# Kernel tuning notes

Hardware: AMD Instinct MI355X
Metric: run time of the kernel (lower is better)

## Reference

```python
import jax, jax.numpy as jnp
import numpy as np

B, G, K, H, NC = 128, 12000, 512, 64, 100
FP = 2048
ALPHA = 0.1
STEPS = 10

def setup_inputs() -> dict:
    key = jax.random.key(0)
    ks = jax.random.split(key, 10)
    ctl = jax.random.normal(ks[0], (B, G), jnp.float32)
    # drug targets: sparse binary indicator per gene
    drug_targets = (jax.random.uniform(ks[1], (B, G)) < 0.01).astype(jnp.float32)
    cell_idx = jax.random.randint(ks[2], (B,), 0, NC, dtype=jnp.int32)
    drug_fp = jax.random.normal(ks[3], (B, FP), jnp.float32)  # unused in forward
    # gene->module membership (sparse-ish binary), ensure each module non-empty via deg clamp in model
    M = (jax.random.uniform(ks[4], (G, K)) < 0.02).astype(jnp.float32)
    # row-stochastic module adjacency for stable diffusion
    Araw = jax.random.uniform(ks[5], (K, K), jnp.float32)
    A = Araw / jnp.sum(Araw, axis=1, keepdims=True)
    W_in = jax.random.normal(ks[6], (2, H), jnp.float32) * 0.5
    b_in = jnp.zeros((H,), jnp.float32)
    cell_emb = jax.random.normal(ks[7], (NC, H), jnp.float32) * 0.02
    W_out = jax.random.normal(ks[8], (H, 1), jnp.float32) * 0.1
    b_out = jnp.zeros((1,), jnp.float32)
    return {"ctl": ctl, "drug_targets": drug_targets, "cell_idx": cell_idx,
            "drug_fp": drug_fp, "M": M, "A": A, "W_in": W_in, "b_in": b_in,
            "cell_emb": cell_emb, "W_out": W_out, "b_out": b_out}

def reference(ctl, drug_targets, cell_idx, drug_fp, M, A, W_in, b_in, cell_emb, W_out, b_out):
    # module degree (clamped) as in __init__
    mod_deg = jnp.maximum(jnp.sum(M, axis=0), 1.0)            # [K]
    x_gene = jnp.stack([ctl, drug_targets], axis=-1)          # [B,G,2]
    x_mod = jnp.einsum('gk,bgh->bkh', M, x_gene) / mod_deg[None, :, None]  # [B,K,2]
    S = jax.nn.relu(x_mod @ W_in + b_in)                      # [B,K,H]
    # 10-step personalized-PageRank-style diffusion over modules
    def step(Z, _):
        Z = (1.0 - ALPHA) * jnp.einsum('bkh,kl->blh', Z, A) + ALPHA * S
        return Z, None
    Z, _ = jax.lax.scan(step, S, None, length=STEPS)          # [B,K,H]
    h_gene = jnp.einsum('gk,bkh->bgh', M, Z)                  # [B,G,H]
    h_gene = h_gene + cell_emb[cell_idx][:, None, :]          # add cell embedding
    y = (h_gene @ W_out + b_out)[..., 0]                      # [B,G]
    return y
```

## Files before the change

kernel.cpp:

```cpp
#include <hip/hip_runtime.h>

#define B_    128
#define G_    12000
#define GP    12288
#define K_    512
#define H_    64
#define NSEG  24
#define SEGG  512
#define BKT   64

typedef __attribute__((ext_vector_type(8))) short bf16x8;
typedef __attribute__((ext_vector_type(4))) float f32x4;

__device__ __forceinline__ unsigned short f2bf(float x) {
    union { float f; unsigned u; } v; v.f = x;
    unsigned r = (v.u + 0x7FFFu + ((v.u >> 16) & 1u)) >> 16;
    return (unsigned short)r;
}
__device__ __forceinline__ float bf2f(unsigned short b) {
    union { float f; unsigned u; } v; v.u = ((unsigned)b) << 16;
    return v.f;
}

__device__ __forceinline__ void mm_body(int k0, int l0, float* __restrict__ sm,
        const float* __restrict__ Aop, const float* __restrict__ Bop,
        const float* __restrict__ Cop, const float* __restrict__ Dop,
        float alpha, float beta, float* __restrict__ O, float* __restrict__ O2) {
    float (*Xa)[68] = (float(*)[68])sm;
    float (*Xb)[36] = (float(*)[36])(sm + 2176);
    int tid = threadIdx.x;
    int kg = tid & 15, lg = tid >> 4;
    float acc[2][2] = {};
    for (int jj = 0; jj < K_; jj += 64) {
#pragma unroll
        for (int i = 0; i < 2; ++i) {
            int lin = tid + i * 256;
            int r = lin >> 4, c4 = lin & 15;
            *(float4*)&Xa[r][c4 * 4] =
                *(const float4*)&Aop[(size_t)(l0 + r) * K_ + jj + c4 * 4];
        }
#pragma unroll
        for (int i = 0; i < 2; ++i) {
            int lin = tid + i * 256;
            int r = lin >> 3, c4 = lin & 7;
            *(float4*)&Xb[r][c4 * 4] =
                *(const float4*)&Bop[(size_t)(jj + r) * K_ + k0 + c4 * 4];
        }
        __syncthreads();
#pragma unroll 8
        for (int j = 0; j < 64; ++j) {
            float xa0 = Xa[lg * 2][j], xa1 = Xa[lg * 2 + 1][j];
            float xb0 = Xb[j][kg * 2], xb1 = Xb[j][kg * 2 + 1];
            acc[0][0] = fmaf(xa0, xb0, acc[0][0]);
            acc[0][1] = fmaf(xa0, xb1, acc[0][1]);
            acc[1][0] = fmaf(xa1, xb0, acc[1][0]);
            acc[1][1] = fmaf(xa1, xb1, acc[1][1]);
        }
        __syncthreads();
    }
#pragma unroll
    for (int i = 0; i < 2; ++i) {
        size_t idx = (size_t)(l0 + lg * 2 + i) * K_ + k0 + kg * 2;
        float2 v;
        v.x = alpha * acc[i][0];
        v.y = alpha * acc[i][1];
        if (beta != 0.0f) {
            float2 cc = *(const float2*)&Cop[idx];
            v.x = fmaf(beta, cc.x, v.x);
            v.y = fmaf(beta, cc.y, v.y);
        }
        *(float2*)&O[idx] = v;
        if (O2) {
            float2 dd = *(const float2*)&Dop[idx];
            float2 w2; w2.x = v.x + dd.x; w2.y = v.y + dd.y;
            *(float2*)&O2[idx] = w2;
        }
    }
}

__global__ __launch_bounds__(256) void k_pre(
        const float* __restrict__ ctl, const float* __restrict__ dt,
        const float* __restrict__ M, const float* __restrict__ A,
        const int* __restrict__ cidx, const float* __restrict__ cemb,
        const float* __restrict__ W_out, const float* __restrict__ b_out,
        unsigned short* __restrict__ XpT, unsigned short* __restrict__ MTb,
        unsigned short* __restrict__ Mb, int* __restrict__ deg,
        float* __restrict__ AT, float* __restrict__ U2,
        float* __restrict__ cvec) {
    int bid = blockIdx.x, tid = threadIdx.x;
    if (bid < 3072) {
        int p = bid / 12, chunk = bid % 12;
        int ch = p >> 7, b = p & 127;
        const float* src = (ch ? dt : ctl) + (size_t)b * G_;
        int g = chunk * 1024 + tid * 4;
        float x0 = 0.f, x1 = 0.f, x2 = 0.f, x3 = 0.f;
        if (g + 3 < G_) {
            float4 v = *(const float4*)&src[g];
            x0 = v.x; x1 = v.y; x2 = v.z; x3 = v.w;
        } else {
            if (g + 0 < G_) x0 = src[g + 0];
            if (g + 1 < G_) x1 = src[g + 1];
            if (g + 2 < G_) x2 = src[g + 2];
            if (g + 3 < G_) x3 = src[g + 3];
        }
        ushort4 hv;
        hv.x = f2bf(x0); hv.y = f2bf(x1); hv.z = f2bf(x2); hv.w = f2bf(x3);
        *(ushort4*)&XpT[(size_t)p * GP + g] = hv;
    } else if (bid < 4608) {
        __shared__ float t[64][65];
        __shared__ int csum[4][64];
        int id = bid - 3072;
        int gt = id % 192, kt = id / 192;
        int g0 = gt * 64, k0 = kt * 64;
        int tx = tid & 63, ty = tid >> 6;
        int cnt = 0;
#pragma unroll
        for (int j = 0; j < 16; ++j) {
            int g = g0 + ty + 4 * j;
            float v = (g < G_) ? M[(size_t)g * K_ + k0 + tx] : 0.0f;
            t[ty + 4 * j][tx] = v;
            Mb[(size_t)g * K_ + k0 + tx] = f2bf(v);
            cnt += (v != 0.0f);
        }
        csum[ty][tx] = cnt;
        __syncthreads();
        if (ty == 0)
            atomicAdd(&deg[k0 + tx],
                      csum[0][tx] + csum[1][tx] + csum[2][tx] + csum[3][tx]);
#pragma unroll
        for (int j = 0; j < 16; ++j)
            MTb[(size_t)(k0 + ty + 4 * j) * GP + g0 + tx] =
                f2bf(t[tx][ty + 4 * j]);
    } else if (bid < 4864) {
        __shared__ float t[32][33];
        int id = bid - 4608;
        int x0 = (id & 15) * 32, y0 = (id >> 4) * 32;
        int tx = tid & 31, ty = tid >> 5;
#pragma unroll
        for (int j = 0; j < 4; ++j)
            t[ty + 8 * j][tx] = A[(size_t)(y0 + ty + 8 * j) * K_ + x0 + tx];
        __syncthreads();
#pragma unroll
        for (int j = 0; j < 4; ++j) {
            int row = x0 + ty + 8 * j, col = y0 + tx;
            float v = t[tx][ty + 8 * j];
            AT[(size_t)row * K_ + col] = v;
            U2[(size_t)row * K_ + col] = 0.09f * v + (row == col ? 0.1f : 0.0f);
        }
    } else {
        if (tid < B_) {
            int ci = cidx[tid];
            float acc = b_out[0];
#pragma unroll 8
            for (int h = 0; h < H_; ++h)
                acc = fmaf(cemb[ci * H_ + h], W_out[h], acc);
            cvec[tid] = acc;
        }
    }
}

__global__ __launch_bounds__(256) void k_gemm(
        const unsigned short* __restrict__ MTb, const unsigned short* __restrict__ XpT,
        float* __restrict__ Cp,
        const float* __restrict__ AT, const float* __restrict__ U2,
        float* __restrict__ M2, float* __restrict__ Yop) {
    __shared__ __align__(16) char smraw[36864];
    int bid = blockIdx.x, tid = threadIdx.x;
    if (bid < 192) {
        unsigned short (*Al)[72] = (unsigned short(*)[72])smraw;
        unsigned short (*Bl)[72] = (unsigned short(*)[72])(smraw + 18432);
        int tile = bid & 7, seg = bid >> 3;
        int m0 = (tile & 3) * 128, n0 = (tile >> 2) * 128;
        size_t gbase = (size_t)seg * SEGG;
        int wid = tid >> 6, lane = tid & 63;
        int wm = (wid >> 1) * 64, wn = (wid & 1) * 64;
        int r16 = lane & 15, kg8 = (lane >> 4) * 8;
        int ld_row = tid >> 3, ld_c8 = (tid & 7) * 8;
        f32x4 acc[4][4] = {};
        for (int kk = 0; kk < SEGG; kk += BKT) {
#pragma unroll
            for (int i = 0; i < 4; ++i) {
                int r = ld_row + 32 * i;
                *(uint4*)&Al[r][ld_c8] =
                    *(const uint4*)&MTb[(size_t)(m0 + r) * GP + gbase + kk + ld_c8];
                *(uint4*)&Bl[r][ld_c8] =
                    *(const uint4*)&XpT[(size_t)(n0 + r) * GP + gbase + kk + ld_c8];
            }
            __syncthreads();
#pragma unroll
            for (int ks = 0; ks < 2; ++ks) {
                bf16x8 af[4], bf[4];
#pragma unroll
                for (int mi = 0; mi < 4; ++mi)
                    af[mi] = *(const bf16x8*)&Al[wm + mi * 16 + r16][ks * 32 + kg8];
#pragma unroll
                for (int ni = 0; ni < 4; ++ni)
                    bf[ni] = *(const bf16x8*)&Bl[wn + ni * 16 + r16][ks * 32 + kg8];
#pragma unroll
                for (int mi = 0; mi < 4; ++mi)
#pragma unroll
                    for (int ni = 0; ni < 4; ++ni)
                        acc[mi][ni] = __builtin_amdgcn_mfma_f32_16x16x32_bf16(
                            af[mi], bf[ni], acc[mi][ni], 0, 0, 0);
            }
            __syncthreads();
        }
        float* C = Cp + (size_t)seg * (K_ * 256);
        int cr = (lane >> 4) * 4, cc = lane & 15;
#pragma unroll
        for (int mi = 0; mi < 4; ++mi)
#pragma unroll
            for (int ni = 0; ni < 4; ++ni) {
                size_t rb = (size_t)(m0 + wm + mi * 16 + cr) * 256
                          + (n0 + wn + ni * 16 + cc);
#pragma unroll
                for (int r = 0; r < 4; ++r)
                    C[rb + (size_t)r * 256] = acc[mi][ni][r];
            }
    } else {
        int id = bid - 192;
        mm_body((id & 15) * 32, (id >> 4) * 32, (float*)smraw,
                AT, AT, nullptr, U2, 0.81f, 0.0f, M2, Yop);
    }
}

__global__ __launch_bounds__(256) void k_red(
        const float* __restrict__ Cp, const int* __restrict__ deg,
        const float* __restrict__ W_in, const float* __restrict__ b_in,
        const float* __restrict__ W_out, float* __restrict__ sout,
        const float* __restrict__ M2, const float* __restrict__ U2,
        float* __restrict__ M4, float* __restrict__ U4) {
    __shared__ __align__(16) float sm[4480];
    int bid = blockIdx.x, tid = threadIdx.x;
    if (bid < 256) {
        int kloc = tid >> 7, b = tid & 127;
        int k = bid * 2 + kloc;
        float x0 = 0.f, x1 = 0.f;
#pragma unroll 4
        for (int s = 0; s < NSEG; ++s) {
            const float* Cb = Cp + (size_t)s * (K_ * 256) + (size_t)k * 256;
            x0 += Cb[b];
            x1 += Cb[128 + b];
        }
        float inv = 1.0f / fmaxf((float)deg[k], 1.0f);
        x0 *= inv; x1 *= inv;
        float s = 0.f;
#pragma unroll 8
        for (int h = 0; h < H_; ++h) {
            float v = fmaf(x0, W_in[h], fmaf(x1, W_in[H_ + h], b_in[h]));
            v = fmaxf(v, 0.f);
            s = fmaf(v, W_out[h], s);
        }
        sout[k * B_ + b] = s;
    } else {
        int id = bid - 256;
        int t = id & 255;
        if (id < 256)
            mm_body((t & 15) * 32, (t >> 4) * 32, sm, M2, M2, nullptr, nullptr,
                    1.0f, 0.0f, M4, nullptr);
        else
            mm_body((t & 15) * 32, (t >> 4) * 32, sm, M2, U2, U2, nullptr,
                    1.0f, 1.0f, U4, nullptr);
    }
}

__global__ __launch_bounds__(256) void k_p3(
        const float* __restrict__ M4, const float* __restrict__ U4,
        float* __restrict__ M8, float* __restrict__ U8,
        const float* __restrict__ Yop, const float* __restrict__ sout,
        float* __restrict__ q) {
    __shared__ __align__(16) float sm[4480];
    int bid = blockIdx.x, tid = threadIdx.x;
    if (bid < 512) {
        int t = bid & 255;
        if (bid < 256)
            mm_body((t & 15) * 32, (t >> 4) * 32, sm, M4, M4, nullptr, nullptr,
                    1.0f, 0.0f, M8, nullptr);
        else
            mm_body((t & 15) * 32, (t >> 4) * 32, sm, M4, U4, U4, nullptr,
                    1.0f, 1.0f, U8, nullptr);
    } else {
        int l = bid - 512;
        float* Wr  = sm;
        float* red = sm + 512;
        if (tid < 128)
            ((float4*)Wr)[tid] = ((const float4*)&Yop[(size_t)l * K_])[tid];
        __syncthreads();
        int b = tid & 127, seg = tid >> 7;
        int kb = seg * 256;
        float a0 = 0.f, a1 = 0.f, a2 = 0.f, a3 = 0.f;
#pragma unroll 4
        for (int kk = 0; kk < 256; kk += 4) {
            int k = kb + kk;
            a0 = fmaf(Wr[k + 0], sout[(k + 0) * B_ + b], a0);
            a1 = fmaf(Wr[k + 1], sout[(k + 1) * B_ + b], a1);
            a2 = fmaf(Wr[k + 2], sout[(k + 2) * B_ + b], a2);
            a3 = fmaf(Wr[k + 3], sout[(k + 3) * B_ + b], a3);
        }
        red[seg * 128 + b] = (a0 + a1) + (a2 + a3);
        __syncthreads();
        if (tid < 128)
            q[l * B_ + b] = red[b] + red[128 + b];
    }
}

__global__ __launch_bounds__(1024) void k_zfin(
        const float* __restrict__ M8, const float* __restrict__ U8,
        const float* __restrict__ q, const float* __restrict__ sout,
        unsigned short* __restrict__ zbT) {
    __shared__ __align__(16) float Wr[4 * K_];
    __shared__ float red[8][2][128];
    int tid = threadIdx.x;
    int l0 = blockIdx.x * 2;
    if (tid < 256)
        ((float4*)Wr)[tid] = ((const float4*)&M8[(size_t)l0 * K_])[tid];
    else if (tid < 512)
        ((float4*)&Wr[2 * K_])[tid - 256] =
            ((const float4*)&U8[(size_t)l0 * K_])[tid - 256];
    __syncthreads();
    int b = tid & 127, seg = tid >> 7;
    int kb = seg * 64;
    float a0m = 0.f, a0u = 0.f, a1m = 0.f, a1u = 0.f;
#pragma unroll 8
    for (int kk = 0; kk < 64; ++kk) {
        int k = kb + kk;
        float qv = q[k * B_ + b];
        float sv = sout[k * B_ + b];
        a0m = fmaf(Wr[k], qv, a0m);
        a0u = fmaf(Wr[2 * K_ + k], sv, a0u);
        a1m = fmaf(Wr[K_ + k], qv, a1m);
        a1u = fmaf(Wr[3 * K_ + k], sv, a1u);
    }
    red[seg][0][b] = a0m + a0u;
    red[seg][1][b] = a1m + a1u;
    __syncthreads();
    if (tid < 256) {
        int row = tid >> 7, bb = tid & 127;
        float t = 0.f;
#pragma unroll
        for (int u = 0; u < 8; ++u) t += red[u][row][bb];
        unsigned short hi = f2bf(t);
        unsigned short lo = f2bf(t - bf2f(hi));
        zbT[(size_t)bb * (2 * K_) + (l0 + row)]      = hi;
        zbT[(size_t)bb * (2 * K_) + K_ + (l0 + row)] = lo;
    }
}

__global__ __launch_bounds__(256) void k_yg(
        const unsigned short* __restrict__ Mb, const unsigned short* __restrict__ zbT,
        const float* __restrict__ cvec, float* __restrict__ y) {
    __shared__ __align__(16) unsigned short Al[128][72];
    __shared__ __align__(16) unsigned short Bh[128][72];
    __shared__ __align__(16) unsigned short Bl2[128][72];
    int tid = threadIdx.x;
    int g0 = blockIdx.x * 128;
    int wid = tid >> 6, lane = tid & 63;
    int wm = (wid >> 1) * 64, wn = (wid & 1) * 64;
    int r16 = lane & 15, kg8 = (lane >> 4) * 8;
    int ld_row = tid >> 3, ld_c8 = (tid & 7) * 8;
    f32x4 acc[4][4] = {};
    for (int kk = 0; kk < K_; kk += BKT) {
#pragma unroll
        for (int i = 0; i < 4; ++i) {
            int r = ld_row + 32 * i;
            *(uint4*)&Al[r][ld_c8] =
                *(const uint4*)&Mb[(size_t)(g0 + r) * K_ + kk + ld_c8];
            *(uint4*)&Bh[r][ld_c8] =
                *(const uint4*)&zbT[(size_t)r * (2 * K_) + kk + ld_c8];
            *(uint4*)&Bl2[r][ld_c8] =
                *(const uint4*)&zbT[(size_t)r * (2 * K_) + K_ + kk + ld_c8];
        }
        __syncthreads();
#pragma unroll
        for (int ks = 0; ks < 2; ++ks) {
            bf16x8 af[4], bh[4], bl[4];
#pragma unroll
            for (int mi = 0; mi < 4; ++mi)
                af[mi] = *(const bf16x8*)&Al[wm + mi * 16 + r16][ks * 32 + kg8];
#pragma unroll
            for (int ni = 0; ni < 4; ++ni) {
                bh[ni] = *(const bf16x8*)&Bh[wn + ni * 16 + r16][ks * 32 + kg8];
                bl[ni] = *(const bf16x8*)&Bl2[wn + ni * 16 + r16][ks * 32 + kg8];
            }
#pragma unroll
            for (int mi = 0; mi < 4; ++mi)
#pragma unroll
                for (int ni = 0; ni < 4; ++ni) {
                    acc[mi][ni] = __builtin_amdgcn_mfma_f32_16x16x32_bf16(
                        af[mi], bh[ni], acc[mi][ni], 0, 0, 0);
                    acc[mi][ni] = __builtin_amdgcn_mfma_f32_16x16x32_bf16(
                        af[mi], bl[ni], acc[mi][ni], 0, 0, 0);
                }
        }
        __syncthreads();
    }
    int cr = (lane >> 4) * 4, cc = lane & 15;
#pragma unroll
    for (int ni = 0; ni < 4; ++ni) {
        int b = wn + ni * 16 + cc;
        float cv = cvec[b];
#pragma unroll
        for (int mi = 0; mi < 4; ++mi) {
            int g = g0 + wm + mi * 16 + cr;
            if (g < G_) {
                float4 o;
                o.x = acc[mi][ni][0] + cv;
                o.y = acc[mi][ni][1] + cv;
                o.z = acc[mi][ni][2] + cv;
                o.w = acc[mi][ni][3] + cv;
                *(float4*)&y[(size_t)b * G_ + g] = o;
            }
        }
    }
}

extern "C" void kernel_launch(void* const* d_in, const int* in_sizes, int n_in,
                              void* d_out, int out_size, void* d_ws, size_t ws_size,
                              hipStream_t stream) {
    const float* ctl   = (const float*)d_in[0];
    const float* dt    = (const float*)d_in[1];
    const int*   cidx  = (const int*)d_in[2];
    const float* M     = (const float*)d_in[4];
    const float* A     = (const float*)d_in[5];
    const float* W_in  = (const float*)d_in[6];
    const float* b_in  = (const float*)d_in[7];
    const float* cemb  = (const float*)d_in[8];
    const float* W_out = (const float*)d_in[9];
    const float* b_out = (const float*)d_in[10];
    float* y = (float*)d_out;

    char* ws = (char*)d_ws;
    size_t o = 0;
    auto take = [&](size_t bytes) { char* p = ws + o; o = (o + bytes + 255) & ~(size_t)255; return p; };
    unsigned short* XpT = (unsigned short*)take((size_t)256 * GP * 2);
    unsigned short* MTb = (unsigned short*)take((size_t)K_ * GP * 2);
    unsigned short* Mb  = (unsigned short*)take((size_t)GP * K_ * 2);
    unsigned short* zbT = (unsigned short*)take((size_t)B_ * 2 * K_ * 2);
    float* Cp   = (float*)take((size_t)NSEG * K_ * 256 * 4);
    int*   deg  = (int*)  take(K_ * 4);
    float* cvec = (float*)take(B_ * 4);
    float* AT   = (float*)take((size_t)K_ * K_ * 4);
    float* U2   = (float*)take((size_t)K_ * K_ * 4);
    float* M2   = (float*)take((size_t)K_ * K_ * 4);
    float* Yop  = (float*)take((size_t)K_ * K_ * 4);
    float* M4   = (float*)take((size_t)K_ * K_ * 4);
    float* U4   = (float*)take((size_t)K_ * K_ * 4);
    float* M8   = (float*)take((size_t)K_ * K_ * 4);
    float* U8   = (float*)take((size_t)K_ * K_ * 4);
    float* sout = (float*)take((size_t)K_ * B_ * 4);
    float* q    = (float*)take((size_t)K_ * B_ * 4);
    (void)ws_size; (void)in_sizes; (void)n_in; (void)out_size;

    hipMemsetAsync(deg, 0, K_ * 4, stream);
    k_pre<<<4865, 256, 0, stream>>>(ctl, dt, M, A, cidx, cemb, W_out, b_out,
                                    XpT, MTb, Mb, deg, AT, U2, cvec);
    k_gemm<<<448, 256, 0, stream>>>(MTb, XpT, Cp, AT, U2, M2, Yop);
    k_red<<<768, 256, 0, stream>>>(Cp, deg, W_in, b_in, W_out, sout,
                                   M2, U2, M4, U4);
    k_p3<<<1024, 256, 0, stream>>>(M4, U4, M8, U8, Yop, sout, q);
    k_zfin<<<K_ / 2, 1024, 0, stream>>>(M8, U8, q, sout, zbT);
    k_yg<<<(G_ + 127) / 128, 256, 0, stream>>>(Mb, zbT, cvec, y);
}
```

Measured before the change: 112.9 us.

## Replace U8 matmul with panel matvec, drop degree atomics, shrink final GEMM tile

The U8 = M4·U4 + U4 matrix-matrix product is replaced by a matrix-vector product (U4 applied to sout), and its result is folded into the final reduction in k_zfin together with M4. The module-degree atomics and the memset are replaced by per-tile partial counts written to a buffer and reduced inside k_red. The output GEMM tile is halved to 64 rows, doubling the number of blocks to improve occupancy across CUs. This trades one 512³ GEMM for cheaper matvecs, at the cost of more partial-degree traffic and a reassociated floating-point sum.

```diff
diff --git a/kernel.cpp b/kernel.cpp
--- a/kernel.cpp
+++ b/kernel.cpp
@@ -8,6 +8,7 @@
 #define NSEG  24
 #define SEGG  512
 #define BKT   64
+#define NGT   192
 
 typedef __attribute__((ext_vector_type(8))) short bf16x8;
 typedef __attribute__((ext_vector_type(4))) float f32x4;
@@ -78,13 +79,39 @@
     }
 }
 
+__device__ __forceinline__ void panel_body(int l, float* __restrict__ sm,
+        const float* __restrict__ W, const float* __restrict__ src,
+        float* __restrict__ out) {
+    float* Wr  = sm;
+    float* red = sm + 512;
+    int tid = threadIdx.x;
+    if (tid < 128)
+        ((float4*)Wr)[tid] = ((const float4*)&W[(size_t)l * K_])[tid];
+    __syncthreads();
+    int b = tid & 127, seg = tid >> 7;
+    int kb = seg * 256;
+    float a0 = 0.f, a1 = 0.f, a2 = 0.f, a3 = 0.f;
+#pragma unroll 4
+    for (int kk = 0; kk < 256; kk += 4) {
+        int k = kb + kk;
+        a0 = fmaf(Wr[k + 0], src[(k + 0) * B_ + b], a0);
+        a1 = fmaf(Wr[k + 1], src[(k + 1) * B_ + b], a1);
+        a2 = fmaf(Wr[k + 2], src[(k + 2) * B_ + b], a2);
+        a3 = fmaf(Wr[k + 3], src[(k + 3) * B_ + b], a3);
+    }
+    red[seg * 128 + b] = (a0 + a1) + (a2 + a3);
+    __syncthreads();
+    if (tid < 128)
+        out[l * B_ + b] = red[b] + red[128 + b];
+}
+
 __global__ __launch_bounds__(256) void k_pre(
         const float* __restrict__ ctl, const float* __restrict__ dt,
         const float* __restrict__ M, const float* __restrict__ A,
         const int* __restrict__ cidx, const float* __restrict__ cemb,
         const float* __restrict__ W_out, const float* __restrict__ b_out,
         unsigned short* __restrict__ XpT, unsigned short* __restrict__ MTb,
-        unsigned short* __restrict__ Mb, int* __restrict__ deg,
+        unsigned short* __restrict__ Mb, int* __restrict__ pdeg,
         float* __restrict__ AT, float* __restrict__ U2,
         float* __restrict__ cvec) {
     int bid = blockIdx.x, tid = threadIdx.x;
@@ -110,7 +137,7 @@
         __shared__ float t[64][65];
         __shared__ int csum[4][64];
         int id = bid - 3072;
-        int gt = id % 192, kt = id / 192;
+        int gt = id % NGT, kt = id / NGT;
         int g0 = gt * 64, k0 = kt * 64;
         int tx = tid & 63, ty = tid >> 6;
         int cnt = 0;
@@ -125,8 +152,8 @@
         csum[ty][tx] = cnt;
         __syncthreads();
         if (ty == 0)
-            atomicAdd(&deg[k0 + tx],
-                      csum[0][tx] + csum[1][tx] + csum[2][tx] + csum[3][tx]);
+            pdeg[(size_t)(k0 + tx) * NGT + gt] =
+                csum[0][tx] + csum[1][tx] + csum[2][tx] + csum[3][tx];
 #pragma unroll
         for (int j = 0; j < 16; ++j)
             MTb[(size_t)(k0 + ty + 4 * j) * GP + g0 + tx] =
@@ -225,7 +252,7 @@
 }
 
 __global__ __launch_bounds__(256) void k_red(
-        const float* __restrict__ Cp, const int* __restrict__ deg,
+        const float* __restrict__ Cp, const int* __restrict__ pdeg,
         const float* __restrict__ W_in, const float* __restrict__ b_in,
         const float* __restrict__ W_out, float* __restrict__ sout,
         const float* __restrict__ M2, const float* __restrict__ U2,
@@ -235,6 +262,17 @@
     if (bid < 256) {
         int kloc = tid >> 7, b = tid & 127;
         int k = bid * 2 + kloc;
+        int v = 0;
+        if (b < 96)
+            v = pdeg[(size_t)k * NGT + b] + pdeg[(size_t)k * NGT + 96 + b];
+#pragma unroll
+        for (int off = 32; off; off >>= 1) v += __shfl_down(v, off, 64);
+        __shared__ int dsum[4];
+        __shared__ float degs[2];
+        if ((tid & 63) == 0) dsum[tid >> 6] = v;
+        __syncthreads();
+        if (tid < 2) degs[tid] = (float)(dsum[tid * 2] + dsum[tid * 2 + 1]);
+        __syncthreads();
         float x0 = 0.f, x1 = 0.f;
 #pragma unroll 4
         for (int s = 0; s < NSEG; ++s) {
@@ -242,14 +280,14 @@
             x0 += Cb[b];
             x1 += Cb[128 + b];
         }
-        float inv = 1.0f / fmaxf((float)deg[k], 1.0f);
+        float inv = 1.0f / fmaxf(degs[kloc], 1.0f);
         x0 *= inv; x1 *= inv;
         float s = 0.f;
 #pragma unroll 8
         for (int h = 0; h < H_; ++h) {
-            float v = fmaf(x0, W_in[h], fmaf(x1, W_in[H_ + h], b_in[h]));
-            v = fmaxf(v, 0.f);
-            s = fmaf(v, W_out[h], s);
+            float vv = fmaf(x0, W_in[h], fmaf(x1, W_in[H_ + h], b_in[h]));
+            vv = fmaxf(vv, 0.f);
+            s = fmaf(vv, W_out[h], s);
         }
         sout[k * B_ + b] = s;
     } else {
@@ -266,47 +304,24 @@
 
 __global__ __launch_bounds__(256) void k_p3(
         const float* __restrict__ M4, const float* __restrict__ U4,
-        float* __restrict__ M8, float* __restrict__ U8,
+        float* __restrict__ M8,
         const float* __restrict__ Yop, const float* __restrict__ sout,
-        float* __restrict__ q) {
+        float* __restrict__ q, float* __restrict__ bb) {
     __shared__ __align__(16) float sm[4480];
-    int bid = blockIdx.x, tid = threadIdx.x;
-    if (bid < 512) {
-        int t = bid & 255;
-        if (bid < 256)
-            mm_body((t & 15) * 32, (t >> 4) * 32, sm, M4, M4, nullptr, nullptr,
-                    1.0f, 0.0f, M8, nullptr);
-        else
-            mm_body((t & 15) * 32, (t >> 4) * 32, sm, M4, U4, U4, nullptr,
-                    1.0f, 1.0f, U8, nullptr);
+    int bid = blockIdx.x;
+    if (bid < 256) {
+        mm_body((bid & 15) * 32, (bid >> 4) * 32, sm, M4, M4, nullptr, nullptr,
+                1.0f, 0.0f, M8, nullptr);
+    } else if (bid < 768) {
+        panel_body(bid - 256, sm, Yop, sout, q);
     } else {
-        int l = bid - 512;
-        float* Wr  = sm;
-        float* red = sm + 512;
-        if (tid < 128)
-            ((float4*)Wr)[tid] = ((const float4*)&Yop[(size_t)l * K_])[tid];
-        __syncthreads();
-        int b = tid & 127, seg = tid >> 7;
-        int kb = seg * 256;
-        float a0 = 0.f, a1 = 0.f, a2 = 0.f, a3 = 0.f;
-#pragma unroll 4
-        for (int kk = 0; kk < 256; kk += 4) {
-            int k = kb + kk;
-            a0 = fmaf(Wr[k + 0], sout[(k + 0) * B_ + b], a0);
-            a1 = fmaf(Wr[k + 1], sout[(k + 1) * B_ + b], a1);
-            a2 = fmaf(Wr[k + 2], sout[(k + 2) * B_ + b], a2);
-            a3 = fmaf(Wr[k + 3], sout[(k + 3) * B_ + b], a3);
-        }
-        red[seg * 128 + b] = (a0 + a1) + (a2 + a3);
-        __syncthreads();
-        if (tid < 128)
-            q[l * B_ + b] = red[b] + red[128 + b];
+        panel_body(bid - 768, sm, U4, sout, bb);
     }
 }
 
 __global__ __launch_bounds__(1024) void k_zfin(
-        const float* __restrict__ M8, const float* __restrict__ U8,
-        const float* __restrict__ q, const float* __restrict__ sout,
+        const float* __restrict__ M8, const float* __restrict__ M4,
+        const float* __restrict__ q, const float* __restrict__ bb,
         unsigned short* __restrict__ zbT) {
     __shared__ __align__(16) float Wr[4 * K_];
     __shared__ float red[8][2][128];
@@ -316,7 +331,7 @@
         ((float4*)Wr)[tid] = ((const float4*)&M8[(size_t)l0 * K_])[tid];
     else if (tid < 512)
         ((float4*)&Wr[2 * K_])[tid - 256] =
-            ((const float4*)&U8[(size_t)l0 * K_])[tid - 256];
+            ((const float4*)&M4[(size_t)l0 * K_])[tid - 256];
     __syncthreads();
     int b = tid & 127, seg = tid >> 7;
     int kb = seg * 64;
@@ -325,46 +340,50 @@
     for (int kk = 0; kk < 64; ++kk) {
         int k = kb + kk;
         float qv = q[k * B_ + b];
-        float sv = sout[k * B_ + b];
+        float bv = bb[k * B_ + b];
         a0m = fmaf(Wr[k], qv, a0m);
-        a0u = fmaf(Wr[2 * K_ + k], sv, a0u);
+        a0u = fmaf(Wr[2 * K_ + k], bv, a0u);
         a1m = fmaf(Wr[K_ + k], qv, a1m);
-        a1u = fmaf(Wr[3 * K_ + k], sv, a1u);
+        a1u = fmaf(Wr[3 * K_ + k], bv, a1u);
     }
     red[seg][0][b] = a0m + a0u;
     red[seg][1][b] = a1m + a1u;
     __syncthreads();
     if (tid < 256) {
-        int row = tid >> 7, bb = tid & 127;
-        float t = 0.f;
-#pragma unroll
-        for (int u = 0; u < 8; ++u) t += red[u][row][bb];
+        int row = tid >> 7, bi = tid & 127;
+        float t = bb[(l0 + row) * B_ + bi];
+#pragma unroll
+        for (int u = 0; u < 8; ++u) t += red[u][row][bi];
         unsigned short hi = f2bf(t);
         unsigned short lo = f2bf(t - bf2f(hi));
-        zbT[(size_t)bb * (2 * K_) + (l0 + row)]      = hi;
-        zbT[(size_t)bb * (2 * K_) + K_ + (l0 + row)] = lo;
+        zbT[(size_t)bi * (2 * K_) + (l0 + row)]      = hi;
+        zbT[(size_t)bi * (2 * K_) + K_ + (l0 + row)] = lo;
     }
 }
 
 __global__ __launch_bounds__(256) void k_yg(
         const unsigned short* __restrict__ Mb, const unsigned short* __restrict__ zbT,
         const float* __restrict__ cvec, float* __restrict__ y) {
-    __shared__ __align__(16) unsigned short Al[128][72];
+    __shared__ __align__(16) unsigned short Al[64][72];
     __shared__ __align__(16) unsigned short Bh[128][72];
     __shared__ __align__(16) unsigned short Bl2[128][72];
     int tid = threadIdx.x;
-    int g0 = blockIdx.x * 128;
+    int g0 = blockIdx.x * 64;
     int wid = tid >> 6, lane = tid & 63;
-    int wm = (wid >> 1) * 64, wn = (wid & 1) * 64;
+    int wm = (wid >> 1) * 32, wn = (wid & 1) * 64;
     int r16 = lane & 15, kg8 = (lane >> 4) * 8;
     int ld_row = tid >> 3, ld_c8 = (tid & 7) * 8;
-    f32x4 acc[4][4] = {};
+    f32x4 acc[2][4] = {};
     for (int kk = 0; kk < K_; kk += BKT) {
 #pragma unroll
-        for (int i = 0; i < 4; ++i) {
+        for (int i = 0; i < 2; ++i) {
             int r = ld_row + 32 * i;
             *(uint4*)&Al[r][ld_c8] =
                 *(const uint4*)&Mb[(size_t)(g0 + r) * K_ + kk + ld_c8];
+        }
+#pragma unroll
+        for (int i = 0; i < 4; ++i) {
+            int r = ld_row + 32 * i;
             *(uint4*)&Bh[r][ld_c8] =
                 *(const uint4*)&zbT[(size_t)r * (2 * K_) + kk + ld_c8];
             *(uint4*)&Bl2[r][ld_c8] =
@@ -373,9 +392,9 @@
         __syncthreads();
 #pragma unroll
         for (int ks = 0; ks < 2; ++ks) {
-            bf16x8 af[4], bh[4], bl[4];
-#pragma unroll
-            for (int mi = 0; mi < 4; ++mi)
+            bf16x8 af[2], bh[4], bl[4];
+#pragma unroll
+            for (int mi = 0; mi < 2; ++mi)
                 af[mi] = *(const bf16x8*)&Al[wm + mi * 16 + r16][ks * 32 + kg8];
 #pragma unroll
             for (int ni = 0; ni < 4; ++ni) {
@@ -383,7 +402,7 @@
                 bl[ni] = *(const bf16x8*)&Bl2[wn + ni * 16 + r16][ks * 32 + kg8];
             }
 #pragma unroll
-            for (int mi = 0; mi < 4; ++mi)
+            for (int mi = 0; mi < 2; ++mi)
 #pragma unroll
                 for (int ni = 0; ni < 4; ++ni) {
                     acc[mi][ni] = __builtin_amdgcn_mfma_f32_16x16x32_bf16(
@@ -400,7 +419,7 @@
         int b = wn + ni * 16 + cc;
         float cv = cvec[b];
 #pragma unroll
-        for (int mi = 0; mi < 4; ++mi) {
+        for (int mi = 0; mi < 2; ++mi) {
             int g = g0 + wm + mi * 16 + cr;
             if (g < G_) {
                 float4 o;
@@ -437,7 +456,7 @@
     unsigned short* Mb  = (unsigned short*)take((size_t)GP * K_ * 2);
     unsigned short* zbT = (unsigned short*)take((size_t)B_ * 2 * K_ * 2);
     float* Cp   = (float*)take((size_t)NSEG * K_ * 256 * 4);
-    int*   deg  = (int*)  take(K_ * 4);
+    int*   pdeg = (int*)  take((size_t)K_ * NGT * 4);
     float* cvec = (float*)take(B_ * 4);
     float* AT   = (float*)take((size_t)K_ * K_ * 4);
     float* U2   = (float*)take((size_t)K_ * K_ * 4);
@@ -446,18 +465,17 @@
     float* M4   = (float*)take((size_t)K_ * K_ * 4);
     float* U4   = (float*)take((size_t)K_ * K_ * 4);
     float* M8   = (float*)take((size_t)K_ * K_ * 4);
-    float* U8   = (float*)take((size_t)K_ * K_ * 4);
     float* sout = (float*)take((size_t)K_ * B_ * 4);
     float* q    = (float*)take((size_t)K_ * B_ * 4);
+    float* bb   = (float*)take((size_t)K_ * B_ * 4);
     (void)ws_size; (void)in_sizes; (void)n_in; (void)out_size;
 
-    hipMemsetAsync(deg, 0, K_ * 4, stream);
     k_pre<<<4865, 256, 0, stream>>>(ctl, dt, M, A, cidx, cemb, W_out, b_out,
-                                    XpT, MTb, Mb, deg, AT, U2, cvec);
+                                    XpT, MTb, Mb, pdeg, AT, U2, cvec);
     k_gemm<<<448, 256, 0, stream>>>(MTb, XpT, Cp, AT, U2, M2, Yop);
-    k_red<<<768, 256, 0, stream>>>(Cp, deg, W_in, b_in, W_out, sout,
+    k_red<<<768, 256, 0, stream>>>(Cp, pdeg, W_in, b_in, W_out, sout,
                                    M2, U2, M4, U4);
-    k_p3<<<1024, 256, 0, stream>>>(M4, U4, M8, U8, Yop, sout, q);
-    k_zfin<<<K_ / 2, 1024, 0, stream>>>(M8, U8, q, sout, zbT);
-    k_yg<<<(G_ + 127) / 128, 256, 0, stream>>>(Mb, zbT, cvec, y);
-}
+    k_p3<<<1280, 256, 0, stream>>>(M4, U4, M8, Yop, sout, q, bb);
+    k_zfin<<<K_ / 2, 1024, 0, stream>>>(M8, M4, q, bb, zbT);
+    k_yg<<<(G_ + 63) / 64, 256, 0, stream>>>(Mb, zbT, cvec, y);
+}
```

After: 98.73 us. 12.5% less time.
